# Performance work log

Hardware: AMD Instinct MI355X
Metric: run time of the kernel (lower is better)

## Reference

```python
import jax, jax.numpy as jnp
import numpy as np

P = 3          # graph partitions
CO = 64        # out_channels
KS = 9         # temporal kernel size (Gamma)
STRIDE = 1     # temporal stride
EPS = 1e-3     # keras BatchNormalization default epsilon


def setup_inputs() -> dict:
    key = jax.random.key(0)
    k1, k2, k3 = jax.random.split(key, 3)
    x = jax.random.normal(k1, (32, 64, 300, 25), dtype=jnp.float32)      # (N, C_in, L, V)
    A = jax.random.uniform(k2, (3, 25, 25), dtype=jnp.float32)           # (P, V, V)
    W = jax.random.normal(k3, (64, 192), dtype=jnp.float32) * 0.05       # (C_in, C_out*P)
    gamma = jnp.ones((64,), dtype=jnp.float32)
    beta = jnp.zeros((64,), dtype=jnp.float32)
    mean = jnp.zeros((64,), dtype=jnp.float32)
    var = jnp.ones((64,), dtype=jnp.float32)
    return {"x": x, "A": A, "W": W, "gamma": gamma, "beta": beta, "mean": mean, "var": var}


def _lt_matrix(L):
    # sum of shifted identities: lt[r, r + i*STRIDE] = 1 for i in [0, KS//STRIDE)
    lt = jnp.zeros((L, L), dtype=jnp.float32)
    for i in range(KS // STRIDE):
        lt = lt + jnp.eye(L, k=i * STRIDE, dtype=jnp.float32)
    return lt


def reference(x, A, W, gamma, beta, mean, var):
    N, C, L, V = x.shape
    res = x  # identity residual (in_channels == out_channels, stride == 1)
    # 1x1 conv: (N,C,L,V) x (C, CO*P) -> (N, CO*P, L, V); channel k = c*P + p (split into CO groups of P)
    y = jnp.einsum('nclv,ck->nklv', x, W)
    y = y.reshape(N, CO, P, L, V)  # (N, C_out, P, L, V)
    # partitioned graph matmul over joints: contract V with A[p]
    z = jnp.einsum('ncplv,pvw->ncplw', y, A)
    # temporal aggregation via handcrafted banded matrix, then sum over partitions
    lt = _lt_matrix(L)
    t = jnp.einsum('ncplv,lm->ncmv', z, lt)  # partition sum fused into einsum
    # BN (inference) over channel axis + ReLU
    inv = gamma / jnp.sqrt(var + EPS)
    xn = (t - mean[None, :, None, None]) * inv[None, :, None, None] + beta[None, :, None, None]
    xn = jax.nn.relu(xn)
    # residual add + final ReLU (dropout is identity at inference)
    return jax.nn.relu(xn + res)
```

## Files before the change

kernel.cpp:

```cpp
#include <hip/hip_runtime.h>
#include <cstdint>
#include <cstddef>

typedef short bf16x8 __attribute__((ext_vector_type(8)));
typedef float f32x4 __attribute__((ext_vector_type(4)));

#define EPS 1e-3f

__device__ __forceinline__ short f32_to_bf16s(float f) {
    union { float f; uint32_t u; } v; v.f = f;
    return (short)((v.u + 0x7FFFu + ((v.u >> 16) & 1u)) >> 16);
}

__global__ __launch_bounds__(256) void prep_kernel(const float* __restrict__ A,
                                                   const float* __restrict__ W,
                                                   unsigned short* __restrict__ wt,
                                                   unsigned short* __restrict__ at) {
    int idx = blockIdx.x * 256 + threadIdx.x;
    if (idx < 12288) {
        int kp = idx >> 6, ci = idx & 63;
        wt[idx] = (unsigned short)f32_to_bf16s(W[ci * 192 + kp]);
    } else {
        int j = idx - 12288;
        if (j < 3072) {
            int w = j / 96, k = j - w * 96;
            float val = 0.f;
            if (w < 25 && k < 75) {
                int p = k / 25, v = k - p * 25;
                val = A[(p * 25 + v) * 25 + w];
            }
            at[j] = (unsigned short)f32_to_bf16s(val);
        }
    }
}

__global__ __launch_bounds__(512, 4) void mega_kernel(
    const float* __restrict__ x,
    const unsigned short* __restrict__ wt,
    const unsigned short* __restrict__ at,
    const float* __restrict__ gamma, const float* __restrict__ beta,
    const float* __restrict__ mean, const float* __restrict__ var,
    float* __restrict__ out) {
    const int ch = blockIdx.x, n = blockIdx.y;
    const int l0 = ch * 8;
    const int tid = threadIdx.x;
    const int wv = tid >> 6, lane = tid & 63, q = lane >> 4, lcol = lane & 15;

    __shared__ __align__(16) short smem[13312];
    __shared__ float scs[64], shs[64];

    bf16x8 b2[2][3];
    #pragma unroll
    for (int nt = 0; nt < 2; ++nt)
        #pragma unroll
        for (int s = 0; s < 3; ++s)
            b2[nt][s] = *(const bf16x8*)(at + (size_t)(nt * 16 + lcol) * 96 + 32 * s + 8 * q);
    if (tid < 64) {
        float sc = gamma[tid] * rsqrtf(var[tid] + EPS);
        scs[tid] = sc;
        shs[tid] = beta[tid] - mean[tid] * sc;
    }

    #pragma unroll 1
    for (int rep = 0; rep < 4; ++rep) {
        int cidx = tid + rep * 512;
        if (cidx < 1600) {
            int ci = cidx / 25, v = cidx - ci * 25;
            const float* xp = x + (size_t)(n * 64 + ci) * 7500 + v;
            float vals[16];
            #pragma unroll
            for (int i = 0; i < 16; ++i) {
                int l = l0 - 8 + i;
                vals[i] = (l >= 0 && l < 300) ? xp[l * 25] : 0.f;
            }
            float run = vals[0] + vals[1] + vals[2] + vals[3]
                      + vals[4] + vals[5] + vals[6] + vals[7];
            short* wb = &smem[(ci >> 3) * 1656 + (ci & 7)];
            #pragma unroll
            for (int j = 0; j < 8; ++j) {
                run += vals[j + 8];
                wb[(j * 25 + v) * 8] = f32_to_bf16s(run);
                run -= vals[j];
            }
        }
    }
    __syncthreads();

    bf16x8 b1[2][2];
    #pragma unroll
    for (int nt = 0; nt < 2; ++nt) {
        int col = wv * 25 + nt * 16 + lcol;
        #pragma unroll
        for (int s = 0; s < 2; ++s)
            b1[nt][s] = *(const bf16x8*)&smem[(4 * s + q) * 1656 + col * 8];
    }
    __syncthreads();

    #pragma unroll
    for (int i = lane; i < 512; i += 64) {
        int r = i >> 5, cc = 72 + (i & 31);
        smem[(wv * 16 + r) * 104 + cc] = 0;
    }

    const int lg = l0 + wv;
    const size_t outrow = ((size_t)n * 64 * 300 + lg) * 25;

    #pragma unroll 1
    for (int g = 0; g < 4; ++g) {
        bf16x8 a1[3][2];
        #pragma unroll
        for (int mt = 0; mt < 3; ++mt)
            #pragma unroll
            for (int s = 0; s < 2; ++s)
                a1[mt][s] = *(const bf16x8*)(wt + (size_t)(g * 48 + mt * 16 + lcol) * 64 + 32 * s + 8 * q);

        f32x4 acc[3][2];
        #pragma unroll
        for (int mt = 0; mt < 3; ++mt)
            #pragma unroll
            for (int nt = 0; nt < 2; ++nt) acc[mt][nt] = (f32x4){0.f, 0.f, 0.f, 0.f};
        #pragma unroll
        for (int s = 0; s < 2; ++s)
            #pragma unroll
            for (int mt = 0; mt < 3; ++mt) {
                bf16x8 av = a1[mt][s];
                #pragma unroll
                for (int nt = 0; nt < 2; ++nt)
                    acc[mt][nt] = __builtin_amdgcn_mfma_f32_16x16x32_bf16(av, b1[nt][s], acc[mt][nt], 0, 0, 0);
            }

        float res[2][4];
        #pragma unroll
        for (int nt = 0; nt < 2; ++nt) {
            int w = nt * 16 + lcol;
            bool val = (w < 25) && (lg < 300);
            #pragma unroll
            for (int r = 0; r < 4; ++r) {
                int c = g * 16 + 4 * q + r;
                res[nt][r] = val ? x[outrow + (size_t)c * 7500 + w] : 0.f;
            }
        }

        #pragma unroll
        for (int mt = 0; mt < 3; ++mt)
            #pragma unroll
            for (int nt = 0; nt < 2; ++nt) {
                int v = nt * 16 + lcol;
                if (v < 25) {
                    #pragma unroll
                    for (int r = 0; r < 4; ++r) {
                        int kpl = mt * 16 + 4 * q + r;
                        int cl = kpl / 3, p = kpl - 3 * cl;
                        smem[(wv * 16 + cl) * 104 + 25 * p + v] = f32_to_bf16s(acc[mt][nt][r]);
                    }
                }
            }

        f32x4 c0 = {0.f, 0.f, 0.f, 0.f}, c1 = {0.f, 0.f, 0.f, 0.f};
        #pragma unroll
        for (int s = 0; s < 3; ++s) {
            bf16x8 a2 = *(const bf16x8*)&smem[(wv * 16 + lcol) * 104 + 32 * s + 8 * q];
            c0 = __builtin_amdgcn_mfma_f32_16x16x32_bf16(a2, b2[0][s], c0, 0, 0, 0);
            c1 = __builtin_amdgcn_mfma_f32_16x16x32_bf16(a2, b2[1][s], c1, 0, 0, 0);
        }

        if (lg < 300) {
            #pragma unroll
            for (int nt = 0; nt < 2; ++nt) {
                int w = nt * 16 + lcol;
                if (w < 25) {
                    f32x4 cc = nt ? c1 : c0;
                    #pragma unroll
                    for (int r = 0; r < 4; ++r) {
                        int c = g * 16 + 4 * q + r;
                        float o = fmaxf(cc[r] * scs[c] + shs[c], 0.f);
                        out[outrow + (size_t)c * 7500 + w] = fmaxf(o + res[nt][r], 0.f);
                    }
                }
            }
        }
    }
}

extern "C" void kernel_launch(void* const* d_in, const int* in_sizes, int n_in,
                              void* d_out, int out_size, void* d_ws, size_t ws_size,
                              hipStream_t stream) {
    const float* x     = (const float*)d_in[0];
    const float* A     = (const float*)d_in[1];
    const float* W     = (const float*)d_in[2];
    const float* gamma = (const float*)d_in[3];
    const float* beta  = (const float*)d_in[4];
    const float* mean  = (const float*)d_in[5];
    const float* var   = (const float*)d_in[6];
    float* out = (float*)d_out;

    char* ws = (char*)d_ws;
    unsigned short* wt = (unsigned short*)ws;
    unsigned short* at = (unsigned short*)(ws + 24576);

    prep_kernel<<<60, 256, 0, stream>>>(A, W, wt, at);
    mega_kernel<<<dim3(38, 32), 512, 0, stream>>>(x, wt, at, gamma, beta, mean, var, out);
}
```

Baseline: 163.5 us.

## Stage x tile into LDS with coalesced float4 loads and reuse it for residual

```diff
diff --git a/kernel.cpp b/kernel.cpp
--- a/kernel.cpp
+++ b/kernel.cpp
@@ -10,6 +10,10 @@
 __device__ __forceinline__ short f32_to_bf16s(float f) {
     union { float f; uint32_t u; } v; v.f = f;
     return (short)((v.u + 0x7FFFu + ((v.u >> 16) & 1u)) >> 16);
+}
+__device__ __forceinline__ float bf16s_to_f32(short s) {
+    union { uint32_t u; float f; } v; v.u = ((uint32_t)(unsigned short)s) << 16;
+    return v.f;
 }
 
 __global__ __launch_bounds__(256) void prep_kernel(const float* __restrict__ A,
@@ -46,7 +50,7 @@
     const int tid = threadIdx.x;
     const int wv = tid >> 6, lane = tid & 63, q = lane >> 4, lcol = lane & 15;
 
-    __shared__ __align__(16) short smem[13312];
+    __shared__ __align__(16) short smem[26112];
     __shared__ float scs[64], shs[64];
 
     bf16x8 b2[2][3];
@@ -61,26 +65,46 @@
         shs[tid] = beta[tid] - mean[tid] * sc;
     }
 
+    {
+        const float* xn = x + (size_t)n * 480000;
+        const int e0 = l0 * 25 - 200;
+        #pragma unroll
+        for (int rep = 0; rep < 13; ++rep) {
+            int i = tid + rep * 512;
+            if (i < 6400) {
+                int ci = i / 100, j = i - ci * 100;
+                int e = e0 + 4 * j;
+                float4 val = make_float4(0.f, 0.f, 0.f, 0.f);
+                if (e >= 0 && e <= 7496)
+                    val = *(const float4*)(xn + (size_t)ci * 7500 + e);
+                short4 sv;
+                sv.x = f32_to_bf16s(val.x); sv.y = f32_to_bf16s(val.y);
+                sv.z = f32_to_bf16s(val.z); sv.w = f32_to_bf16s(val.w);
+                int dst = (j < 50) ? (ci * 204 + 4 * j) : (13056 + ci * 204 + 4 * j - 200);
+                *(short4*)&smem[dst] = sv;
+            }
+        }
+    }
+    __syncthreads();
+
     #pragma unroll 1
     for (int rep = 0; rep < 4; ++rep) {
         int cidx = tid + rep * 512;
         if (cidx < 1600) {
             int ci = cidx / 25, v = cidx - ci * 25;
-            const float* xp = x + (size_t)(n * 64 + ci) * 7500 + v;
-            float vals[16];
-            #pragma unroll
-            for (int i = 0; i < 16; ++i) {
-                int l = l0 - 8 + i;
-                vals[i] = (l >= 0 && l < 300) ? xp[l * 25] : 0.f;
-            }
-            float run = vals[0] + vals[1] + vals[2] + vals[3]
-                      + vals[4] + vals[5] + vals[6] + vals[7];
-            short* wb = &smem[(ci >> 3) * 1656 + (ci & 7)];
+            short* hp = &smem[ci * 204 + v];
+            const short* bp = &smem[13056 + ci * 204 + v];
+            float hv[8], bv[8];
+            #pragma unroll
+            for (int j = 0; j < 8; ++j) hv[j] = bf16s_to_f32(hp[j * 25]);
+            #pragma unroll
+            for (int j = 0; j < 8; ++j) bv[j] = bf16s_to_f32(bp[j * 25]);
+            float run = hv[0] + hv[1] + hv[2] + hv[3] + hv[4] + hv[5] + hv[6] + hv[7];
             #pragma unroll
             for (int j = 0; j < 8; ++j) {
-                run += vals[j + 8];
-                wb[(j * 25 + v) * 8] = f32_to_bf16s(run);
-                run -= vals[j];
+                run += bv[j];
+                hp[j * 25] = f32_to_bf16s(run);
+                run -= hv[j];
             }
         }
     }
@@ -91,15 +115,20 @@
     for (int nt = 0; nt < 2; ++nt) {
         int col = wv * 25 + nt * 16 + lcol;
         #pragma unroll
-        for (int s = 0; s < 2; ++s)
-            b1[nt][s] = *(const bf16x8*)&smem[(4 * s + q) * 1656 + col * 8];
+        for (int s = 0; s < 2; ++s) {
+            bf16x8 f;
+            #pragma unroll
+            for (int j = 0; j < 8; ++j)
+                f[j] = smem[(32 * s + 8 * q + j) * 204 + col];
+            b1[nt][s] = f;
+        }
     }
     __syncthreads();
 
     #pragma unroll
-    for (int i = lane; i < 512; i += 64) {
-        int r = i >> 5, cc = 72 + (i & 31);
-        smem[(wv * 16 + r) * 104 + cc] = 0;
+    for (int i = lane; i < 336; i += 64) {
+        int r = i / 21, kk = 75 + (i - r * 21);
+        smem[(wv * 16 + r) * 96 + kk] = 0;
     }
 
     const int lg = l0 + wv;
@@ -128,18 +157,6 @@
                 for (int nt = 0; nt < 2; ++nt)
                     acc[mt][nt] = __builtin_amdgcn_mfma_f32_16x16x32_bf16(av, b1[nt][s], acc[mt][nt], 0, 0, 0);
             }
-
-        float res[2][4];
-        #pragma unroll
-        for (int nt = 0; nt < 2; ++nt) {
-            int w = nt * 16 + lcol;
-            bool val = (w < 25) && (lg < 300);
-            #pragma unroll
-            for (int r = 0; r < 4; ++r) {
-                int c = g * 16 + 4 * q + r;
-                res[nt][r] = val ? x[outrow + (size_t)c * 7500 + w] : 0.f;
-            }
-        }
 
         #pragma unroll
         for (int mt = 0; mt < 3; ++mt)
@@ -151,7 +168,7 @@
                     for (int r = 0; r < 4; ++r) {
                         int kpl = mt * 16 + 4 * q + r;
                         int cl = kpl / 3, p = kpl - 3 * cl;
-                        smem[(wv * 16 + cl) * 104 + 25 * p + v] = f32_to_bf16s(acc[mt][nt][r]);
+                        smem[(wv * 16 + cl) * 96 + 25 * p + v] = f32_to_bf16s(acc[mt][nt][r]);
                     }
                 }
             }
@@ -159,7 +176,7 @@
         f32x4 c0 = {0.f, 0.f, 0.f, 0.f}, c1 = {0.f, 0.f, 0.f, 0.f};
         #pragma unroll
         for (int s = 0; s < 3; ++s) {
-            bf16x8 a2 = *(const bf16x8*)&smem[(wv * 16 + lcol) * 104 + 32 * s + 8 * q];
+            bf16x8 a2 = *(const bf16x8*)&smem[(wv * 16 + lcol) * 96 + 32 * s + 8 * q];
             c0 = __builtin_amdgcn_mfma_f32_16x16x32_bf16(a2, b2[0][s], c0, 0, 0, 0);
             c1 = __builtin_amdgcn_mfma_f32_16x16x32_bf16(a2, b2[1][s], c1, 0, 0, 0);
         }
@@ -173,8 +190,9 @@
                     #pragma unroll
                     for (int r = 0; r < 4; ++r) {
                         int c = g * 16 + 4 * q + r;
+                        float res = bf16s_to_f32(smem[13056 + c * 204 + wv * 25 + w]);
                         float o = fmaxf(cc[r] * scs[c] + shs[c], 0.f);
-                        out[outrow + (size_t)c * 7500 + w] = fmaxf(o + res[nt][r], 0.f);
+                        out[outrow + (size_t)c * 7500 + w] = fmaxf(o + res, 0.f);
                     }
                 }
             }
```

Measured after the change: 172.1 us. 5.3% more time.
